# Optimization experiments

Measured on AMD Instinct MI355X. Metric: run time of the kernel, lower is better.

The kernel has to match this reference:

```python
import jax, jax.numpy as jnp
import numpy as np

IMAGE_H, IMAGE_W = 256, 704
Z, Y, X = 128, 8, 128
BOUNDS = (-50.0, 50.0, -5.0, 5.0, -50.0, 50.0)
CENTROID = (0.0, 1.0, 0.0)
EPS_MEAN = 1e-6
EPS_DEPTH = 1e-4


def _compose_rt(R, t):
    M = jnp.zeros(R.shape[:-2] + (4, 4), R.dtype)
    M = M.at[..., :3, :3].set(R)
    M = M.at[..., :3, 3].set(t)
    M = M.at[..., 3, 3].set(1.0)
    return M


def _safe_inverse(M):
    R = M[..., :3, :3]
    t = M[..., :3, 3]
    Rt = jnp.swapaxes(R, -1, -2)
    return _compose_rt(Rt, -jnp.einsum('...ij,...j->...i', Rt, t))


def _apply_4x4(M, xyz):
    # M: (...,4,4), xyz: (...,N,3) -> (...,N,3)
    return jnp.einsum('...ij,...nj->...ni', M[..., :3, :3], xyz) + M[..., None, :3, 3]


def _xyz_camA():
    # Mem2Ref of gridcloud3d: x_ref = x_mem*vox + MIN + vox/2 (bounds shifted by centroid)
    xmin = BOUNDS[0] + CENTROID[0]; xmax = BOUNDS[1] + CENTROID[0]
    ymin = BOUNDS[2] + CENTROID[1]; ymax = BOUNDS[3] + CENTROID[1]
    zmin = BOUNDS[4] + CENTROID[2]; zmax = BOUNDS[5] + CENTROID[2]
    vx = (xmax - xmin) / X; vy = (ymax - ymin) / Y; vz = (zmax - zmin) / Z
    zz, yy, xx = jnp.meshgrid(jnp.arange(Z, dtype=jnp.float32),
                              jnp.arange(Y, dtype=jnp.float32),
                              jnp.arange(X, dtype=jnp.float32), indexing='ij')
    x = xx * vx + xmin + vx / 2.0
    y = yy * vy + ymin + vy / 2.0
    z = zz * vz + zmin + vz / 2.0
    return jnp.stack([x, y, z], -1).reshape(Z * Y * X, 3)  # mem order (Z,Y,X)


def _bilinear_sample(img, px, py):
    # img: (C,H,W); px,py: (N,) pixel coords; zeros padding (grid_sample align_corners=False)
    C, H, W = img.shape
    x0 = jnp.floor(px); y0 = jnp.floor(py)
    dx = px - x0; dy = py - y0
    x0i = x0.astype(jnp.int32); y0i = y0.astype(jnp.int32)
    flat = img.reshape(C, H * W)

    def gather(yi, xi, w):
        inb = (xi >= 0) & (xi < W) & (yi >= 0) & (yi < H)
        idx = jnp.clip(yi, 0, H - 1) * W + jnp.clip(xi, 0, W - 1)
        return flat[:, idx] * (w * inb.astype(img.dtype))

    return (gather(y0i, x0i, (1 - dx) * (1 - dy))
            + gather(y0i, x0i + 1, dx * (1 - dy))
            + gather(y0i + 1, x0i, (1 - dx) * dy)
            + gather(y0i + 1, x0i + 1, dx * dy))  # (C,N)


def _forward(cam_feat, camera2ego, cam_intrinsic, conv_w):
    B, S, C, Hf, Wf = cam_feat.shape
    # velo_T_cams = merge_rt(camera2ego R, t); cam0_T_camXs = inv(velo_T_cams[:,0]) @ velo_T_cams
    velo_T_cams = _compose_rt(camera2ego[..., :3, :3], camera2ego[..., :3, 3])
    cam0_T_velo = _safe_inverse(velo_T_cams[:, 0])
    cam0_T_camXs = jnp.einsum('bij,bsjk->bsik', cam0_T_velo, velo_T_cams)
    camXs_T_cam0 = _safe_inverse(cam0_T_camXs)
    # scale_intrinsics with sy = Hf/H*0.284, sx = Wf/W*0.44
    sy = Hf / float(IMAGE_H) * 0.284
    sx = Wf / float(IMAGE_W) * 0.44
    fx = cam_intrinsic[..., 0, 0] * sx
    fy = cam_intrinsic[..., 1, 1] * sy
    cx = cam_intrinsic[..., 0, 2] * sx
    cy = cam_intrinsic[..., 1, 2] * sy
    K = jnp.zeros((B, S, 4, 4), cam_feat.dtype)
    K = K.at[..., 0, 0].set(fx).at[..., 1, 1].set(fy)
    K = K.at[..., 0, 2].set(cx).at[..., 1, 2].set(cy)
    K = K.at[..., 2, 2].set(1.0).at[..., 3, 3].set(1.0)
    pixB_T_cam0 = jnp.einsum('bsij,bsjk->bsik', K, camXs_T_cam0)

    xyz = _xyz_camA()  # (N,3), N = Z*Y*X
    xyz_camB = _apply_4x4(camXs_T_cam0, xyz[None, None])  # (B,S,N,3)
    z_cam = xyz_camB[..., 2]
    xyz_pix = _apply_4x4(pixB_T_cam0, xyz[None, None])
    depth = jnp.maximum(xyz_pix[..., 2], EPS_DEPTH)
    x_pix = xyz_pix[..., 0] / depth
    y_pix = xyz_pix[..., 1] / depth
    valid = ((x_pix > -0.5) & (x_pix < Wf - 0.5)
             & (y_pix > -0.5) & (y_pix < Hf - 0.5)
             & (z_cam > 0.0)).astype(cam_feat.dtype)
    # normalize_grid2d (clamp [-2,2]) then grid_sample align_corners=False unnormalize
    gx = jnp.clip(2.0 * x_pix / (Wf - 1) - 1.0, -2.0, 2.0)
    gy = jnp.clip(2.0 * y_pix / (Hf - 1) - 1.0, -2.0, 2.0)
    px = ((gx + 1.0) * Wf - 1.0) / 2.0
    py = ((gy + 1.0) * Hf - 1.0) / 2.0

    feats = cam_feat.reshape(B * S, C, Hf, Wf)
    vals = jax.vmap(_bilinear_sample)(feats, px.reshape(B * S, -1), py.reshape(B * S, -1))
    vals = vals.reshape(B, S, C, -1) * valid[:, :, None, :]  # (B,S,C,N)
    mask = (jnp.abs(vals) > 0).astype(vals.dtype)
    feat_mem = jnp.sum(vals * mask, axis=1) / (EPS_MEAN + jnp.sum(mask, axis=1))  # (B,C,N)
    feat_mem = feat_mem.reshape(B, C, Z, Y, X)

    # BEV compress: permute(0,1,3,2,4) -> (B, C*Y, Z, X), conv3x3 (no bias), InstanceNorm2d, GELU
    feat_bev = jnp.transpose(feat_mem, (0, 1, 3, 2, 4)).reshape(B, C * Y, Z, X)
    out = jax.lax.conv_general_dilated(feat_bev, conv_w, (1, 1), ((1, 1), (1, 1)),
                                       dimension_numbers=('NCHW', 'OIHW', 'NCHW'))
    mu = jnp.mean(out, axis=(2, 3), keepdims=True)
    var = jnp.var(out, axis=(2, 3), keepdims=True)
    out = (out - mu) / jnp.sqrt(var + 1e-5)
    return jax.nn.gelu(out, approximate=False)


def setup_inputs() -> dict:
    key = jax.random.key(0)
    k1, k2, k3 = jax.random.split(key, 3)
    B, S, C, Hf, Wf = 1, 6, 128, 32, 88
    cam_feat = jax.random.normal(k1, (B, S, C, Hf, Wf), jnp.float32)
    # rigid camera2ego: yaw rotations about the y axis + small translations
    yaws = jnp.arange(S, dtype=jnp.float32) * (2.0 * jnp.pi / S)
    c, s = jnp.cos(yaws), jnp.sin(yaws)
    zr, on = jnp.zeros_like(c), jnp.ones_like(c)
    R = jnp.stack([jnp.stack([c, zr, s], -1),
                   jnp.stack([zr, on, zr], -1),
                   jnp.stack([-s, zr, c], -1)], -2)  # (S,3,3)
    t = jax.random.normal(k2, (S, 3), jnp.float32) * 0.5
    cam2ego = jnp.zeros((B, S, 4, 4), jnp.float32)
    cam2ego = cam2ego.at[0, :, :3, :3].set(R).at[0, :, :3, 3].set(t).at[0, :, 3, 3].set(1.0)
    K = jnp.zeros((B, S, 4, 4), jnp.float32)
    K = K.at[..., 0, 0].set(600.0).at[..., 1, 1].set(600.0)
    K = K.at[..., 0, 2].set(352.0).at[..., 1, 2].set(128.0)
    K = K.at[..., 2, 2].set(1.0).at[..., 3, 3].set(1.0)
    conv_w = jax.random.normal(k3, (128, 128 * Y, 3, 3), jnp.float32) / np.sqrt(128 * Y * 9.0).astype(np.float32)
    return {"cam_feat": cam_feat, "camera2ego": cam2ego, "cam_intrinsic": K, "conv_w": conv_w}


def reference(cam_feat, camera2ego, cam_intrinsic, conv_w):
    return _forward(cam_feat, camera2ego, cam_intrinsic, conv_w)
```

## Files before the change

### kernel.cpp

```cpp
#include <hip/hip_runtime.h>
#include <hip/hip_bf16.h>
#include <math.h>

#define HF 32
#define WF 88
#define NCAM 6
#define CC 128
#define ZD 128
#define YD 8
#define XD 128

using f32x4  = __attribute__((ext_vector_type(4))) float;
using bf16x8 = __attribute__((ext_vector_type(8))) short;

#define OFF_P    0ull
#define OFF_W    512ull
#define OFF_CAMT (OFF_W + 2359296ull)
#define OFF_F    (OFF_CAMT + 8650752ull)
#define OFF_CONV (OFF_F + 34611200ull)

__global__ __launch_bounds__(64) void k0_mats(const float* __restrict__ cam2ego,
                                              const float* __restrict__ intr,
                                              float* __restrict__ P) {
  int s = threadIdx.x;
  if (s >= NCAM) return;
  const float* M0 = cam2ego;
  const float* Ms = cam2ego + s * 16;
  float Rb[9], tb[3];
  for (int i = 0; i < 3; i++)
    for (int j = 0; j < 3; j++) {
      float v = 0.f;
      for (int k = 0; k < 3; k++) v += Ms[k * 4 + i] * M0[k * 4 + j];
      Rb[i * 3 + j] = v;
    }
  for (int i = 0; i < 3; i++) {
    float v = 0.f;
    for (int k = 0; k < 3; k++) v += Ms[k * 4 + i] * (M0[k * 4 + 3] - Ms[k * 4 + 3]);
    tb[i] = v;
  }
  const float* Ks = intr + s * 16;
  const float sx = (float)WF / 704.0f * 0.44f;
  const float sy = (float)HF / 256.0f * 0.284f;
  const float fx = Ks[0] * sx, fy = Ks[5] * sy;
  const float cx = Ks[2] * sx, cy = Ks[6] * sy;
  float* p = P + s * 12;
  for (int j = 0; j < 3; j++) p[j]     = fx * Rb[j]     + cx * Rb[6 + j];
  p[3]  = fx * tb[0] + cx * tb[2];
  for (int j = 0; j < 3; j++) p[4 + j] = fy * Rb[3 + j] + cy * Rb[6 + j];
  p[7]  = fy * tb[1] + cy * tb[2];
  for (int j = 0; j < 3; j++) p[8 + j] = Rb[6 + j];
  p[11] = tb[2];
}

__global__ __launch_bounds__(128) void k1_transpose(const float* __restrict__ feat,
                                                    __hip_bfloat16* __restrict__ camT) {
  const int b = blockIdx.x;
  const int wq = b & 3;
  const int sh = b >> 2;
  const int c = threadIdx.x;
  const float* src = feat + ((size_t)(sh / HF) * CC + c) * (HF * WF) + (sh % HF) * WF + wq * 22;
  __hip_bfloat16* dst = camT + ((size_t)sh * WF + wq * 22) * CC + c;
  for (int w = 0; w < 22; w++) dst[w * CC] = __float2bfloat16(src[w]);
}

__global__ __launch_bounds__(256) void k1b_packw(const float* __restrict__ w,
                                                 __hip_bfloat16* __restrict__ wp) {
  const int t = blockIdx.x * 256 + threadIdx.x;
  float v[9];
  #pragma unroll
  for (int d = 0; d < 9; d++) v[d] = w[(size_t)t * 9 + d];
  #pragma unroll
  for (int d = 0; d < 9; d++) wp[(size_t)d * 131072 + t] = __float2bfloat16(v[d]);
}

struct Rec { int off[4]; float w[4]; };

__global__ __launch_bounds__(256) void k2_sample(const __hip_bfloat16* __restrict__ camT,
                                                 const float* __restrict__ P,
                                                 __hip_bfloat16* __restrict__ F) {
  const int bz = blockIdx.x / 130;
  const int bx = blockIdx.x % 130;
  const int t = threadIdx.x;
  const int zi = bz - 1, xi = bx - 1;
  const int c = (t & 63) << 1;
  const int yq = t >> 6;
  __hip_bfloat16* Fb = F + (size_t)blockIdx.x * 1024;
  if (zi < 0 || zi >= ZD || xi < 0 || xi >= XD) {
    *reinterpret_cast<unsigned*>(Fb + c * 8 + yq * 2) = 0u;
    *reinterpret_cast<unsigned*>(Fb + (c + 1) * 8 + yq * 2) = 0u;
    return;
  }
  __shared__ Rec recs[48];
  __shared__ unsigned ymask[8];
  bool vflag = false;
  if (t < 48) {
    const int y = t / 6, s = t - y * 6;
    const float* pp = P + s * 12;
    const float vx = 100.0f / 128.0f;
    const float xw = xi * vx - 50.0f + vx * 0.5f;
    const float zw = zi * vx - 50.0f + vx * 0.5f;
    const float yw = y * 1.25f - 4.0f + 0.625f;
    const float zc = pp[8] * xw + pp[9] * yw + pp[10] * zw + pp[11];
    const float xp = pp[0] * xw + pp[1] * yw + pp[2] * zw + pp[3];
    const float yp = pp[4] * xw + pp[5] * yw + pp[6] * zw + pp[7];
    const float dep = fmaxf(zc, 1e-4f);
    const float pxf = xp / dep, pyf = yp / dep;
    const bool valid = (pxf > -0.5f && pxf < (float)WF - 0.5f &&
                        pyf > -0.5f && pyf < (float)HF - 0.5f && zc > 0.0f);
    const float px = pxf * ((float)WF / (float)(WF - 1)) - 0.5f;
    const float py = pyf * ((float)HF / (float)(HF - 1)) - 0.5f;
    const float fx0 = floorf(px), fy0 = floorf(py);
    const float ddx = px - fx0, ddy = py - fy0;
    const int x0i = (int)fx0, y0i = (int)fy0;
    const float vf = valid ? 1.0f : 0.0f;
    float ww[4];
    ww[0] = (1.0f - ddx) * (1.0f - ddy) * vf;
    ww[1] = ddx * (1.0f - ddy) * vf;
    ww[2] = (1.0f - ddx) * ddy * vf;
    ww[3] = ddx * ddy * vf;
    const int cxs[4] = {x0i, x0i + 1, x0i, x0i + 1};
    const int cys[4] = {y0i, y0i, y0i + 1, y0i + 1};
    Rec r;
    float wsum = 0.f;
    #pragma unroll
    for (int k = 0; k < 4; k++) {
      const bool inb = ((unsigned)cxs[k] < WF) && ((unsigned)cys[k] < HF);
      const int xc = min(max(cxs[k], 0), WF - 1);
      const int yc = min(max(cys[k], 0), HF - 1);
      r.w[k] = inb ? ww[k] : 0.0f;
      r.off[k] = (s * (HF * WF) + yc * WF + xc) * CC;
      wsum += r.w[k];
    }
    recs[t] = r;
    vflag = wsum > 0.0f;
  }
  if (t < 64) {
    unsigned long long m = __ballot(vflag);
    if (t < 8) ymask[t] = (unsigned)((m >> (6 * t)) & 63ull);
  }
  __syncthreads();

  float num[2][2] = {{0.f, 0.f}, {0.f, 0.f}};
  int cnt[2] = {0, 0};
  #pragma unroll
  for (int yi = 0; yi < 2; yi++) {
    const int y = yq * 2 + yi;
    unsigned ms = ymask[y];
    while (ms) {
      const int s = __builtin_ctz(ms);
      ms &= ms - 1;
      const Rec r = recs[y * 6 + s];
      float v0 = 0.f, v1 = 0.f;
      #pragma unroll
      for (int k = 0; k < 4; k++) {
        const ushort2 uv = *reinterpret_cast<const ushort2*>(&camT[r.off[k] + c]);
        v0 += r.w[k] * __bfloat162float(*reinterpret_cast<const __hip_bfloat16*>(&uv.x));
        v1 += r.w[k] * __bfloat162float(*reinterpret_cast<const __hip_bfloat16*>(&uv.y));
      }
      num[yi][0] += v0;
      num[yi][1] += v1;
      cnt[yi]++;
    }
  }
  #pragma unroll
  for (int j = 0; j < 2; j++) {
    __hip_bfloat16 o[2];
    const float inv0 = 1.0f / (1e-6f + (float)cnt[0]);
    const float inv1 = 1.0f / (1e-6f + (float)cnt[1]);
    o[0] = __float2bfloat16(num[0][j] * inv0);
    o[1] = __float2bfloat16(num[1][j] * inv1);
    *reinterpret_cast<unsigned*>(Fb + (c + j) * 8 + yq * 2) =
        *reinterpret_cast<const unsigned*>(o);
  }
}

__device__ __forceinline__ void load_lds16(const void* g, void* l) {
  __builtin_amdgcn_global_load_lds(
      (const __attribute__((address_space(1))) unsigned int*)g,
      (__attribute__((address_space(3))) unsigned int*)l, 16, 0, 0);
}

#define K3_NT 72

__global__ __launch_bounds__(512) void k3_gemm(const __hip_bfloat16* __restrict__ F,
                                               const __hip_bfloat16* __restrict__ Wp,
                                               float* __restrict__ out0,
                                               float* __restrict__ out1) {
  const int orig = (blockIdx.x & 7) * 32 + (blockIdx.x >> 3);
  const int z = orig & 127;
  const int h = orig >> 7;
  const int ciH = h << 9;
  const int tid = threadIdx.x;
  const int w = tid >> 6;
  const int l = tid & 63;
  const int kk = w >> 2;
  const int wq = w & 3;
  const int wm = wq >> 1;
  const int wn = wq & 1;
  __shared__ __hip_bfloat16 lds[4][16384];

  f32x4 acc[4][4];
  #pragma unroll
  for (int m = 0; m < 4; m++)
    #pragma unroll
    for (int n = 0; n < 4; n++)
      acc[m][n] = (f32x4){0.f, 0.f, 0.f, 0.f};

  auto stage = [&](int kt) {
    const int buf = kt & 3;
    const int d = kt >> 3;
    const int dz = d / 3, dx = d - dz * 3;
    const int ci0 = ciH + ((kt & 7) << 6);
    const int zbase = (z + dz) * 130 + dx;
    #pragma unroll
    for (int i = 0; i < 2; i++) {
      const int n = w * 128 + i * 64 + l;
      const int row = n >> 3;
      const int q = (n & 7) ^ (row & 7);
      const __hip_bfloat16* src = F + ((size_t)(zbase + row) << 10) + ci0 + (q << 3);
      load_lds16(src, &lds[buf][(w * 128 + i * 64) * 8]);
    }
    #pragma unroll
    for (int i = 0; i < 2; i++) {
      const int n = w * 128 + i * 64 + l;
      const int co = n >> 3;
      const int q = (n & 7) ^ (co & 7);
      const __hip_bfloat16* src = Wp + ((size_t)d << 17) + ((size_t)co << 10) + ci0 + (q << 3);
      load_lds16(src, &lds[buf][8192 + (w * 128 + i * 64) * 8]);
    }
  };

  auto compute = [&](int kt) {
    const int buf = kt & 3;
    const int r16 = l & 15;
    const int hi = l >> 4;
    const int c = kk * 4 + hi;
    bf16x8 a[4], b[4];
    #pragma unroll
    for (int m = 0; m < 4; m++) {
      const int r = wm * 64 + m * 16 + r16;
      const int slot = c ^ (r & 7);
      a[m] = *reinterpret_cast<const bf16x8*>(&lds[buf][r * 64 + slot * 8]);
    }
    #pragma unroll
    for (int n = 0; n < 4; n++) {
      const int co = wn * 64 + n * 16 + r16;
      const int slot = c ^ (co & 7);
      b[n] = *reinterpret_cast<const bf16x8*>(&lds[buf][8192 + co * 64 + slot * 8]);
    }
    #pragma unroll
    for (int m = 0; m < 4; m++)
      #pragma unroll
      for (int n = 0; n < 4; n++)
        acc[m][n] = __builtin_amdgcn_mfma_f32_16x16x32_bf16(a[m], b[n], acc[m][n], 0, 0, 0);
  };

  stage(0); stage(1); stage(2);

  for (int t = 0; t < K3_NT - 2; ++t) {
    asm volatile("s_waitcnt vmcnt(8)" ::: "memory");
    __builtin_amdgcn_s_barrier();
    if (t + 3 < K3_NT) stage(t + 3);
    compute(t);
  }
  asm volatile("s_waitcnt vmcnt(4)" ::: "memory");
  __builtin_amdgcn_s_barrier();
  compute(K3_NT - 2);
  asm volatile("s_waitcnt vmcnt(0)" ::: "memory");
  __builtin_amdgcn_s_barrier();
  compute(K3_NT - 1);

  float* red = reinterpret_cast<float*>(&lds[0][0]);
  if (kk == 1) {
    float* dst = red + wq * 4096;
    #pragma unroll
    for (int m = 0; m < 4; m++)
      #pragma unroll
      for (int n = 0; n < 4; n++)
        *reinterpret_cast<f32x4*>(&dst[(m * 4 + n) * 256 + l * 4]) = acc[m][n];
  }
  __syncthreads();
  if (kk == 0) {
    const float* srcr = red + wq * 4096;
    float* outP = h ? out1 : out0;
    const int r16 = l & 15;
    const int hi = l >> 4;
    #pragma unroll
    for (int m = 0; m < 4; m++) {
      const int xr = wm * 64 + m * 16 + hi * 4;
      #pragma unroll
      for (int n = 0; n < 4; n++) {
        f32x4 o = *reinterpret_cast<const f32x4*>(&srcr[(m * 4 + n) * 256 + l * 4]);
        f32x4 r = acc[m][n] + o;
        const int co = wn * 64 + n * 16 + r16;
        *reinterpret_cast<f32x4*>(&outP[((size_t)co << 14) + (z << 7) + xr]) = r;
      }
    }
  }
}

__device__ __forceinline__ float gelu_exact(float x) {
  return 0.5f * x * (1.0f + erff(x * 0.70710678118654752440f));
}

__global__ __launch_bounds__(1024) void k4_ln(const float* __restrict__ c0,
                                              const float* __restrict__ c1,
                                              float* __restrict__ outp) {
  const int co = blockIdx.x;
  const int t = threadIdx.x;
  const float4* p0 = reinterpret_cast<const float4*>(c0 + ((size_t)co << 14));
  const float4* p1 = reinterpret_cast<const float4*>(c1 + ((size_t)co << 14));
  float4 v[4];
  float s = 0.f, s2 = 0.f;
  #pragma unroll
  for (int i = 0; i < 4; i++) {
    float4 a = p0[t + (i << 10)];
    float4 b = p1[t + (i << 10)];
    float4 r;
    r.x = a.x + b.x; r.y = a.y + b.y; r.z = a.z + b.z; r.w = a.w + b.w;
    v[i] = r;
    s  += r.x + r.y + r.z + r.w;
    s2 += r.x * r.x + r.y * r.y + r.z * r.z + r.w * r.w;
  }
  #pragma unroll
  for (int off = 32; off > 0; off >>= 1) {
    s  += __shfl_down(s, off);
    s2 += __shfl_down(s2, off);
  }
  __shared__ float red[32];
  __shared__ float mb[2];
  const int wv = t >> 6, ln = t & 63;
  if (ln == 0) { red[wv] = s; red[wv + 16] = s2; }
  __syncthreads();
  if (t == 0) {
    float S = 0.f, S2 = 0.f;
    #pragma unroll
    for (int i = 0; i < 16; i++) { S += red[i]; S2 += red[i + 16]; }
    float mu = S * (1.0f / 16384.0f);
    float var = S2 * (1.0f / 16384.0f) - mu * mu;
    mb[0] = mu;
    mb[1] = 1.0f / sqrtf(var + 1e-5f);
  }
  __syncthreads();
  const float mu = mb[0], inv = mb[1];
  float4* op = reinterpret_cast<float4*>(outp + ((size_t)co << 14));
  #pragma unroll
  for (int i = 0; i < 4; i++) {
    float4 x = v[i];
    float4 r;
    r.x = gelu_exact((x.x - mu) * inv);
    r.y = gelu_exact((x.y - mu) * inv);
    r.z = gelu_exact((x.z - mu) * inv);
    r.w = gelu_exact((x.w - mu) * inv);
    op[t + (i << 10)] = r;
  }
}

extern "C" void kernel_launch(void* const* d_in, const int* in_sizes, int n_in,
                              void* d_out, int out_size, void* d_ws, size_t ws_size,
                              hipStream_t stream) {
  const float* cam_feat = (const float*)d_in[0];
  const float* cam2ego  = (const float*)d_in[1];
  const float* intr     = (const float*)d_in[2];
  const float* conv_w   = (const float*)d_in[3];
  float* out = (float*)d_out;
  char* ws = (char*)d_ws;

  float*          P     = (float*)(ws + OFF_P);
  __hip_bfloat16* Wp    = (__hip_bfloat16*)(ws + OFF_W);
  __hip_bfloat16* camT  = (__hip_bfloat16*)(ws + OFF_CAMT);
  __hip_bfloat16* F     = (__hip_bfloat16*)(ws + OFF_F);
  float*          conv0 = (float*)(ws + OFF_CONV);
  float*          conv1 = (float*)(ws + OFF_CAMT);

  hipLaunchKernelGGL(k0_mats, dim3(1), dim3(64), 0, stream, cam2ego, intr, P);
  hipLaunchKernelGGL(k1_transpose, dim3(NCAM * HF * 4), dim3(128), 0, stream, cam_feat, camT);
  hipLaunchKernelGGL(k1b_packw, dim3(512), dim3(256), 0, stream, conv_w, Wp);
  hipLaunchKernelGGL(k2_sample, dim3(130 * 130), dim3(256), 0, stream, camT, P, F);
  hipLaunchKernelGGL(k3_gemm, dim3(256), dim3(512), 0, stream, F, Wp, conv0, conv1);
  hipLaunchKernelGGL(k4_ln, dim3(128), dim3(1024), 0, stream, conv0, conv1, out);
}
```

Before: 109.7 us.

## Tile camera transpose through LDS and widen sampling loads to four channels

The camera-feature transpose now stages a whole 128x88 row in shared memory (padded stride 89), so global reads and bf16 writes are both coalesced instead of strided per channel. The sampling kernel packs two x-columns per 256-thread block, with each thread handling four channels via 8-byte loads instead of two via 4-byte loads. This halves the block count and cuts per-channel load instructions in the gather. It costs more registers per thread and about 45KB of LDS for the transpose, and the transpose runs only 192 blocks.

```diff
diff --git a/kernel.cpp b/kernel.cpp
--- a/kernel.cpp
+++ b/kernel.cpp
@@ -52,15 +52,26 @@
   p[11] = tb[2];
 }
 
-__global__ __launch_bounds__(128) void k1_transpose(const float* __restrict__ feat,
+__global__ __launch_bounds__(256) void k1_transpose(const float* __restrict__ feat,
                                                     __hip_bfloat16* __restrict__ camT) {
+  __shared__ float tile[128 * 89];
   const int b = blockIdx.x;
-  const int wq = b & 3;
-  const int sh = b >> 2;
-  const int c = threadIdx.x;
-  const float* src = feat + ((size_t)(sh / HF) * CC + c) * (HF * WF) + (sh % HF) * WF + wq * 22;
-  __hip_bfloat16* dst = camT + ((size_t)sh * WF + wq * 22) * CC + c;
-  for (int w = 0; w < 22; w++) dst[w * CC] = __float2bfloat16(src[w]);
+  const int s = b >> 5;
+  const int hrow = b & 31;
+  const int t = threadIdx.x;
+  for (int idx = t; idx < 128 * 88; idx += 256) {
+    const int c = idx / 88;
+    const int w = idx - c * 88;
+    tile[c * 89 + w] = feat[((size_t)(s * CC + c) * HF + hrow) * WF + w];
+  }
+  __syncthreads();
+  const int c = t & 127;
+  const int wh = t >> 7;
+  for (int i = 0; i < 44; i++) {
+    const int w = i * 2 + wh;
+    camT[((size_t)(s * HF + hrow) * WF + w) * CC + c] =
+        __float2bfloat16(tile[c * 89 + w]);
+  }
 }
 
 __global__ __launch_bounds__(256) void k1b_packw(const float* __restrict__ w,
@@ -78,23 +89,25 @@
 __global__ __launch_bounds__(256) void k2_sample(const __hip_bfloat16* __restrict__ camT,
                                                  const float* __restrict__ P,
                                                  __hip_bfloat16* __restrict__ F) {
-  const int bz = blockIdx.x / 130;
-  const int bx = blockIdx.x % 130;
+  const int bz = blockIdx.x / 65;
+  const int bxp = blockIdx.x % 65;
   const int t = threadIdx.x;
+  const int sub = t >> 7;
+  const int u = t & 127;
+  const int bx = bxp * 2 + sub;
   const int zi = bz - 1, xi = bx - 1;
-  const int c = (t & 63) << 1;
-  const int yq = t >> 6;
-  __hip_bfloat16* Fb = F + (size_t)blockIdx.x * 1024;
-  if (zi < 0 || zi >= ZD || xi < 0 || xi >= XD) {
-    *reinterpret_cast<unsigned*>(Fb + c * 8 + yq * 2) = 0u;
-    *reinterpret_cast<unsigned*>(Fb + (c + 1) * 8 + yq * 2) = 0u;
-    return;
-  }
-  __shared__ Rec recs[48];
-  __shared__ unsigned ymask[8];
+  const int cq = (u & 31) << 2;
+  const int yq = u >> 5;
+  __hip_bfloat16* Fb = F + ((size_t)bz * 130 + bx) * 1024;
+  const bool inplay = !(zi < 0 || zi >= ZD || xi < 0 || xi >= XD);
+
+  __shared__ Rec recs[2][48];
+  __shared__ unsigned ymask[2][8];
+  const int lane = t & 63;
+  const int wv = t >> 6;
   bool vflag = false;
-  if (t < 48) {
-    const int y = t / 6, s = t - y * 6;
+  if ((wv == 0 || wv == 2) && lane < 48 && inplay) {
+    const int y = lane / 6, s = lane - y * 6;
     const float* pp = P + s * 12;
     const float vx = 100.0f / 128.0f;
     const float xw = xi * vx - 50.0f + vx * 0.5f;
@@ -131,45 +144,51 @@
       r.off[k] = (s * (HF * WF) + yc * WF + xc) * CC;
       wsum += r.w[k];
     }
-    recs[t] = r;
+    recs[sub][lane] = r;
     vflag = wsum > 0.0f;
   }
-  if (t < 64) {
+  if (wv == 0 || wv == 2) {
     unsigned long long m = __ballot(vflag);
-    if (t < 8) ymask[t] = (unsigned)((m >> (6 * t)) & 63ull);
+    if (lane < 8) ymask[wv >> 1][lane] = (unsigned)((m >> (6 * lane)) & 63ull);
   }
   __syncthreads();
 
-  float num[2][2] = {{0.f, 0.f}, {0.f, 0.f}};
+  if (!inplay) {
+    #pragma unroll
+    for (int j = 0; j < 4; j++)
+      *reinterpret_cast<unsigned*>(Fb + (cq + j) * 8 + yq * 2) = 0u;
+    return;
+  }
+
+  float num[2][4] = {{0.f, 0.f, 0.f, 0.f}, {0.f, 0.f, 0.f, 0.f}};
   int cnt[2] = {0, 0};
   #pragma unroll
   for (int yi = 0; yi < 2; yi++) {
     const int y = yq * 2 + yi;
-    unsigned ms = ymask[y];
+    unsigned ms = ymask[sub][y];
     while (ms) {
       const int s = __builtin_ctz(ms);
       ms &= ms - 1;
-      const Rec r = recs[y * 6 + s];
-      float v0 = 0.f, v1 = 0.f;
+      const Rec r = recs[sub][y * 6 + s];
       #pragma unroll
       for (int k = 0; k < 4; k++) {
-        const ushort2 uv = *reinterpret_cast<const ushort2*>(&camT[r.off[k] + c]);
-        v0 += r.w[k] * __bfloat162float(*reinterpret_cast<const __hip_bfloat16*>(&uv.x));
-        v1 += r.w[k] * __bfloat162float(*reinterpret_cast<const __hip_bfloat16*>(&uv.y));
+        const ushort4 uv = *reinterpret_cast<const ushort4*>(&camT[r.off[k] + cq]);
+        num[yi][0] += r.w[k] * __bfloat162float(*reinterpret_cast<const __hip_bfloat16*>(&uv.x));
+        num[yi][1] += r.w[k] * __bfloat162float(*reinterpret_cast<const __hip_bfloat16*>(&uv.y));
+        num[yi][2] += r.w[k] * __bfloat162float(*reinterpret_cast<const __hip_bfloat16*>(&uv.z));
+        num[yi][3] += r.w[k] * __bfloat162float(*reinterpret_cast<const __hip_bfloat16*>(&uv.w));
       }
-      num[yi][0] += v0;
-      num[yi][1] += v1;
       cnt[yi]++;
     }
   }
-  #pragma unroll
-  for (int j = 0; j < 2; j++) {
+  const float inv0 = 1.0f / (1e-6f + (float)cnt[0]);
+  const float inv1 = 1.0f / (1e-6f + (float)cnt[1]);
+  #pragma unroll
+  for (int j = 0; j < 4; j++) {
     __hip_bfloat16 o[2];
-    const float inv0 = 1.0f / (1e-6f + (float)cnt[0]);
-    const float inv1 = 1.0f / (1e-6f + (float)cnt[1]);
     o[0] = __float2bfloat16(num[0][j] * inv0);
     o[1] = __float2bfloat16(num[1][j] * inv1);
-    *reinterpret_cast<unsigned*>(Fb + (c + j) * 8 + yq * 2) =
+    *reinterpret_cast<unsigned*>(Fb + (cq + j) * 8 + yq * 2) =
         *reinterpret_cast<const unsigned*>(o);
   }
 }
@@ -374,9 +393,9 @@
   float*          conv1 = (float*)(ws + OFF_CAMT);
 
   hipLaunchKernelGGL(k0_mats, dim3(1), dim3(64), 0, stream, cam2ego, intr, P);
-  hipLaunchKernelGGL(k1_transpose, dim3(NCAM * HF * 4), dim3(128), 0, stream, cam_feat, camT);
+  hipLaunchKernelGGL(k1_transpose, dim3(NCAM * HF), dim3(256), 0, stream, cam_feat, camT);
   hipLaunchKernelGGL(k1b_packw, dim3(512), dim3(256), 0, stream, conv_w, Wp);
-  hipLaunchKernelGGL(k2_sample, dim3(130 * 130), dim3(256), 0, stream, camT, P, F);
+  hipLaunchKernelGGL(k2_sample, dim3(130 * 65), dim3(256), 0, stream, camT, P, F);
   hipLaunchKernelGGL(k3_gemm, dim3(256), dim3(512), 0, stream, F, Wp, conv0, conv1);
   hipLaunchKernelGGL(k4_ln, dim3(128), dim3(1024), 0, stream, conv0, conv1, out);
 }
```

After: 111.1 us. Within noise of the previous version (+1.3%).
